# Optimization experiments

Hardware: AMD Instinct MI355X
Metric: run time of the kernel (lower is better)

The kernel has to match this reference:

```python
import jax, jax.numpy as jnp
import numpy as np

EPS = 1e-6  # cosine-similarity eps, as in pytorch3d chamfer_distance


def setup_inputs() -> dict:
    key = jax.random.key(0)
    k1, k2, k3, k4 = jax.random.split(key, 4)
    B, N, M, D = 4, 8192, 8192, 3
    return {
        "xyz1": jax.random.normal(k1, (B, N, D), dtype=jnp.float32),
        "xyz2": jax.random.normal(k2, (B, M, D), dtype=jnp.float32),
        "nxyz1": jax.random.normal(k3, (B, N, D), dtype=jnp.float32),
        "nxyz2": jax.random.normal(k4, (B, M, D), dtype=jnp.float32),
    }


def _pairwise_sqdist(x, y):
    # x: [B,N,D], y: [B,M,D] -> [B,N,M] squared euclidean distances
    x2 = jnp.sum(x * x, axis=-1)  # [B,N]
    y2 = jnp.sum(y * y, axis=-1)  # [B,M]
    xy = jnp.einsum("bnd,bmd->bnm", x, y)
    return x2[:, :, None] + y2[:, None, :] - 2.0 * xy


def _cos_sim(a, b):
    # cosine similarity along last axis with norm clamping (torch F.cosine_similarity style)
    na = jnp.maximum(jnp.linalg.norm(a, axis=-1), EPS)
    nb = jnp.maximum(jnp.linalg.norm(b, axis=-1), EPS)
    return jnp.sum(a * b, axis=-1) / (na * nb)


def reference(xyz1, xyz2, nxyz1, nxyz2):
    # pytorch3d chamfer_distance, point_reduction='mean', batch_reduction='mean'
    d = _pairwise_sqdist(xyz1, xyz2)          # [B,N,M]
    cham_x = jnp.min(d, axis=2)               # [B,N] nearest y for each x
    idx_x = jnp.argmin(d, axis=2)             # [B,N]
    cham_y = jnp.min(d, axis=1)               # [B,M] nearest x for each y
    idx_y = jnp.argmin(d, axis=1)             # [B,M]

    # point mean then batch mean == overall mean
    cham_dist = jnp.mean(cham_x) + jnp.mean(cham_y)

    # normal consistency: gather nearest-neighbor normals via argmin indices
    ny_for_x = jnp.take_along_axis(nxyz2, idx_x[:, :, None], axis=1)  # [B,N,3]
    nx_for_y = jnp.take_along_axis(nxyz1, idx_y[:, :, None], axis=1)  # [B,M,3]
    cham_norm_x = 1.0 - jnp.abs(_cos_sim(nxyz1, ny_for_x))            # [B,N]
    cham_norm_y = 1.0 - jnp.abs(_cos_sim(nxyz2, nx_for_y))            # [B,M]
    cham_normals = jnp.mean(cham_norm_x) + jnp.mean(cham_norm_y)

    return cham_dist, cham_normals
```

## Files before the change

kernel.cpp:

```cpp
#include <hip/hip_runtime.h>

#define CH_EPS 1e-6f
#define NPTS 8192
#define NB 4
#define NSEG 8
#define SEGSZ (NPTS / NSEG)
#define TILE 32
#define NTILE (SEGSZ / TILE)
#define CHSZ 16
#define NQT 4
#define QPW (32 * NQT)
#define QPB (4 * QPW)
#define NQ_TOT (2 * NB * NPTS)
#define BIGF 3.0e38f
#define CHMASK 0xFFFFFE00u

typedef _Float16 half8 __attribute__((ext_vector_type(8)));
typedef float floatx16 __attribute__((ext_vector_type(16)));

__device__ __forceinline__ unsigned mono(float f) {
    unsigned b = __float_as_uint(f);
    return (b & 0x80000000u) ? ~b : (b | 0x80000000u);
}
__device__ __forceinline__ unsigned mono_inv(unsigned u) {
    return (u & 0x80000000u) ? (u & 0x7FFFFFFFu) : ~u;
}

__global__ __launch_bounds__(256) void chamfer_partial(
    const float* __restrict__ xyz1, const float* __restrict__ xyz2,
    unsigned* __restrict__ part, float* __restrict__ out) {
    __shared__ half8 sA[SEGSZ + 1];

    const int tid = threadIdx.x;
    const int chq = blockIdx.x;
    const int seg = blockIdx.y;
    const int db = blockIdx.z;
    const int dir = db >> 2, b = db & 3;

    if (chq == 0 && seg == 0 && db == 0 && tid < 2) out[tid] = 0.0f;

    const float* Q = dir ? xyz2 : xyz1;
    const float* R = (dir ? xyz1 : xyz2) + ((size_t)b * NPTS + seg * SEGSZ) * 3;

    for (int k = tid; k < SEGSZ; k += 256) {
        float a = R[3 * k], c = R[3 * k + 1], e = R[3 * k + 2];
        float h = 0.5f * fmaf(a, a, fmaf(c, c, e * e));
        half8 v = {(_Float16)a, (_Float16)c, (_Float16)e, (_Float16)h,
                   (_Float16)0, (_Float16)0, (_Float16)0, (_Float16)0};
        sA[k] = v;
    }
    if (tid == 0) {
        half8 z = {(_Float16)0, (_Float16)0, (_Float16)0, (_Float16)0,
                   (_Float16)0, (_Float16)0, (_Float16)0, (_Float16)0};
        sA[SEGSZ] = z;
    }

    const int wave = tid >> 6, lane = tid & 63;
    const int n = lane & 31;
    const bool lohalf = lane < 32;
    const int qbase = chq * QPB + wave * QPW;

    half8 bfrag[NQT];
    float best[NQT];
#pragma unroll
    for (int qt = 0; qt < NQT; ++qt) {
        half8 v = {(_Float16)0, (_Float16)0, (_Float16)0, (_Float16)0,
                   (_Float16)0, (_Float16)0, (_Float16)0, (_Float16)0};
        if (lohalf) {
            const size_t off = ((size_t)b * NPTS + qbase + qt * 32 + n) * 3;
            v[0] = (_Float16)(-Q[off]);
            v[1] = (_Float16)(-Q[off + 1]);
            v[2] = (_Float16)(-Q[off + 2]);
            v[3] = (_Float16)1.0f;
        }
        bfrag[qt] = v;
        best[qt] = BIGF;
    }
    __syncthreads();

    const floatx16 zacc = {0};
    const unsigned gt0 = seg * NTILE;

    for (int rt = 0; rt < NTILE; ++rt) {
        const half8 af = sA[lohalf ? (rt * TILE + n) : SEGSZ];
        const unsigned gcl = (gt0 + rt) * 2;

        floatx16 d[NQT];
#pragma unroll
        for (int qt = 0; qt < NQT; ++qt)
            d[qt] = __builtin_amdgcn_mfma_f32_32x32x16_f16(
                af, bfrag[qt], zacc, 0, 0, 0);

#pragma unroll
        for (int qt = 0; qt < NQT; ++qt) {
            float lo = fminf(fminf(fminf(d[qt][0], d[qt][1]), fminf(d[qt][2], d[qt][3])),
                             fminf(fminf(d[qt][4], d[qt][5]), fminf(d[qt][6], d[qt][7])));
            float hi = fminf(fminf(fminf(d[qt][8], d[qt][9]), fminf(d[qt][10], d[qt][11])),
                             fminf(fminf(d[qt][12], d[qt][13]), fminf(d[qt][14], d[qt][15])));
            float kl = __uint_as_float((__float_as_uint(lo) & CHMASK) | gcl);
            float kh = __uint_as_float((__float_as_uint(hi) & CHMASK) | (gcl + 1));
            best[qt] = fminf(best[qt], fminf(kl, kh));
        }
    }

    const int qg = dir * (NB * NPTS) + b * NPTS + qbase;
#pragma unroll
    for (int qt = 0; qt < NQT; ++qt) {
        float v = best[qt];
        v = fminf(v, __shfl_xor(v, 32));
        if (lohalf) atomicMin(&part[qg + qt * 32 + n], mono(v));
    }
}

__global__ __launch_bounds__(256) void finalize_kernel(
    const float* __restrict__ xyz1, const float* __restrict__ xyz2,
    const float* __restrict__ nxyz1, const float* __restrict__ nxyz2,
    const unsigned* __restrict__ part, float* __restrict__ out) {
    __shared__ float red[2][4];

    const int tid = threadIdx.x;
    const int q = blockIdx.x * 256 + tid;
    const int dir = q >> 15;
    const int rem = q & 32767;
    const int b = rem >> 13;
    const int i = rem & 8191;

    const int c = (int)(mono_inv(part[q]) & 0x1FFu);

    const float* Q   = dir ? xyz2 : xyz1;
    const float* Rf  = dir ? xyz1 : xyz2;
    const float* NQp = dir ? nxyz2 : nxyz1;
    const float* NRp = dir ? nxyz1 : nxyz2;

    const size_t qoff = ((size_t)b * NPTS + i) * 3;
    const float x0 = Q[qoff], x1 = Q[qoff + 1], x2 = Q[qoff + 2];
    const float n0 = -x0, n1 = -x1, n2 = -x2;

    const float4* Rs = (const float4*)(Rf + ((size_t)b * NPTS + c * CHSZ) * 3);
    float btr = BIGF;
    int bj = 0;
#pragma unroll
    for (int g = 0; g < 4; ++g) {
        const float4 f0 = Rs[3 * g];
        const float4 f1 = Rs[3 * g + 1];
        const float4 f2 = Rs[3 * g + 2];
        const float px[4] = {f0.x, f0.w, f1.z, f2.y};
        const float py[4] = {f0.y, f1.x, f1.w, f2.z};
        const float pz[4] = {f0.z, f1.y, f2.x, f2.w};
#pragma unroll
        for (int u = 0; u < 4; ++u) {
            float h = 0.5f * fmaf(px[u], px[u], fmaf(py[u], py[u], pz[u] * pz[u]));
            float t = fmaf(n0, px[u], fmaf(n1, py[u], fmaf(n2, pz[u], h)));
            int j = 4 * g + u;
            if (t < btr) { btr = t; bj = j; }
        }
    }
    const int bi = c * CHSZ + bj;

    const size_t roff = ((size_t)b * NPTS + bi) * 3;
    const float y0 = Rf[roff], y1 = Rf[roff + 1], y2 = Rf[roff + 2];
    const float e0 = x0 - y0, e1 = x1 - y1, e2 = x2 - y2;
    float d = e0 * e0 + e1 * e1 + e2 * e2;

    const float a0 = NQp[qoff], a1 = NQp[qoff + 1], a2 = NQp[qoff + 2];
    const float c0 = NRp[roff], c1 = NRp[roff + 1], c2 = NRp[roff + 2];
    float na = sqrtf(a0 * a0 + a1 * a1 + a2 * a2);
    float nc = sqrtf(c0 * c0 + c1 * c1 + c2 * c2);
    float cs = (a0 * c0 + a1 * c1 + a2 * c2) /
               (fmaxf(na, CH_EPS) * fmaxf(nc, CH_EPS));
    float cn = 1.0f - fabsf(cs);

    for (int off = 32; off; off >>= 1) {
        d  += __shfl_down(d, off);
        cn += __shfl_down(cn, off);
    }
    const int lane = tid & 63, wv = tid >> 6;
    if (lane == 0) { red[0][wv] = d; red[1][wv] = cn; }
    __syncthreads();
    if (tid == 0) {
        float sd = red[0][0] + red[0][1] + red[0][2] + red[0][3];
        float sc = red[1][0] + red[1][1] + red[1][2] + red[1][3];
        const float inv = 1.0f / (float)(NB * NPTS);
        atomicAdd(out + 0, sd * inv);
        atomicAdd(out + 1, sc * inv);
    }
}

extern "C" void kernel_launch(void* const* d_in, const int* in_sizes, int n_in,
                              void* d_out, int out_size, void* d_ws, size_t ws_size,
                              hipStream_t stream) {
    const float* xyz1  = (const float*)d_in[0];
    const float* xyz2  = (const float*)d_in[1];
    const float* nxyz1 = (const float*)d_in[2];
    const float* nxyz2 = (const float*)d_in[3];
    float* out = (float*)d_out;
    unsigned* part = (unsigned*)d_ws;

    hipMemsetAsync(part, 0xFF, (size_t)NQ_TOT * sizeof(unsigned), stream);
    chamfer_partial<<<dim3(NPTS / QPB, NSEG, 2 * NB), dim3(256), 0, stream>>>(
        xyz1, xyz2, part, out);
    finalize_kernel<<<dim3(NQ_TOT / 256), dim3(256), 0, stream>>>(
        xyz1, xyz2, nxyz1, nxyz2, part, out);
}
```

Measured before the change: 106.0 us.

## Store per-segment partial minima instead of atomics; use 32-point chunk keys

Each segment now writes its per-query minimum key to its own slice of the workspace. The finalize kernel reduces the 16 slices itself, which removes the memset and the global atomicMin. Segments double to 16 for more blocks, and each key now encodes a 32-point chunk with an 8-bit index, folding both 32-row halves of the MFMA tile into a single min. The finalize kernel must now rescan 32 candidates per query and read 16 partial values, and the workspace grows by 16x. Negative distance keys still compare correctly under fminf.

After: 104.1 us. No clear change (-1.7%).

```diff
diff --git a/kernel.cpp b/kernel.cpp
--- a/kernel.cpp
+++ b/kernel.cpp
@@ -3,32 +3,24 @@
 #define CH_EPS 1e-6f
 #define NPTS 8192
 #define NB 4
-#define NSEG 8
+#define NSEG 16
 #define SEGSZ (NPTS / NSEG)
 #define TILE 32
 #define NTILE (SEGSZ / TILE)
-#define CHSZ 16
+#define CHSZ 32
 #define NQT 4
 #define QPW (32 * NQT)
 #define QPB (4 * QPW)
 #define NQ_TOT (2 * NB * NPTS)
 #define BIGF 3.0e38f
-#define CHMASK 0xFFFFFE00u
+#define CHMASK 0xFFFFFF00u
 
 typedef _Float16 half8 __attribute__((ext_vector_type(8)));
 typedef float floatx16 __attribute__((ext_vector_type(16)));
 
-__device__ __forceinline__ unsigned mono(float f) {
-    unsigned b = __float_as_uint(f);
-    return (b & 0x80000000u) ? ~b : (b | 0x80000000u);
-}
-__device__ __forceinline__ unsigned mono_inv(unsigned u) {
-    return (u & 0x80000000u) ? (u & 0x7FFFFFFFu) : ~u;
-}
-
 __global__ __launch_bounds__(256) void chamfer_partial(
     const float* __restrict__ xyz1, const float* __restrict__ xyz2,
-    unsigned* __restrict__ part, float* __restrict__ out) {
+    float* __restrict__ part, float* __restrict__ out) {
     __shared__ half8 sA[SEGSZ + 1];
 
     const int tid = threadIdx.x;
@@ -79,27 +71,22 @@
     __syncthreads();
 
     const floatx16 zacc = {0};
-    const unsigned gt0 = seg * NTILE;
+    const unsigned gc0 = seg * NTILE;
 
     for (int rt = 0; rt < NTILE; ++rt) {
         const half8 af = sA[lohalf ? (rt * TILE + n) : SEGSZ];
-        const unsigned gcl = (gt0 + rt) * 2;
-
-        floatx16 d[NQT];
-#pragma unroll
-        for (int qt = 0; qt < NQT; ++qt)
-            d[qt] = __builtin_amdgcn_mfma_f32_32x32x16_f16(
-                af, bfrag[qt], zacc, 0, 0, 0);
-
+        const unsigned gc = gc0 + rt;
 #pragma unroll
         for (int qt = 0; qt < NQT; ++qt) {
-            float lo = fminf(fminf(fminf(d[qt][0], d[qt][1]), fminf(d[qt][2], d[qt][3])),
-                             fminf(fminf(d[qt][4], d[qt][5]), fminf(d[qt][6], d[qt][7])));
-            float hi = fminf(fminf(fminf(d[qt][8], d[qt][9]), fminf(d[qt][10], d[qt][11])),
-                             fminf(fminf(d[qt][12], d[qt][13]), fminf(d[qt][14], d[qt][15])));
-            float kl = __uint_as_float((__float_as_uint(lo) & CHMASK) | gcl);
-            float kh = __uint_as_float((__float_as_uint(hi) & CHMASK) | (gcl + 1));
-            best[qt] = fminf(best[qt], fminf(kl, kh));
+            floatx16 d = __builtin_amdgcn_mfma_f32_32x32x16_f16(
+                af, bfrag[qt], zacc, 0, 0, 0);
+            float m0 = fminf(fminf(d[0], d[1]), fminf(d[2], d[3]));
+            float m1 = fminf(fminf(d[4], d[5]), fminf(d[6], d[7]));
+            float m2 = fminf(fminf(d[8], d[9]), fminf(d[10], d[11]));
+            float m3 = fminf(fminf(d[12], d[13]), fminf(d[14], d[15]));
+            float mn = fminf(fminf(m0, m1), fminf(m2, m3));
+            float key = __uint_as_float((__float_as_uint(mn) & CHMASK) | gc);
+            best[qt] = fminf(best[qt], key);
         }
     }
 
@@ -108,14 +95,14 @@
     for (int qt = 0; qt < NQT; ++qt) {
         float v = best[qt];
         v = fminf(v, __shfl_xor(v, 32));
-        if (lohalf) atomicMin(&part[qg + qt * 32 + n], mono(v));
+        if (lohalf) part[(size_t)seg * NQ_TOT + qg + qt * 32 + n] = v;
     }
 }
 
 __global__ __launch_bounds__(256) void finalize_kernel(
     const float* __restrict__ xyz1, const float* __restrict__ xyz2,
     const float* __restrict__ nxyz1, const float* __restrict__ nxyz2,
-    const unsigned* __restrict__ part, float* __restrict__ out) {
+    const float* __restrict__ part, float* __restrict__ out) {
     __shared__ float red[2][4];
 
     const int tid = threadIdx.x;
@@ -125,7 +112,10 @@
     const int b = rem >> 13;
     const int i = rem & 8191;
 
-    const int c = (int)(mono_inv(part[q]) & 0x1FFu);
+    float bt = part[q];
+#pragma unroll
+    for (int s = 1; s < NSEG; ++s) bt = fminf(bt, part[(size_t)s * NQ_TOT + q]);
+    const int c = (int)(__float_as_uint(bt) & 0xFFu);
 
     const float* Q   = dir ? xyz2 : xyz1;
     const float* Rf  = dir ? xyz1 : xyz2;
@@ -140,7 +130,7 @@
     float btr = BIGF;
     int bj = 0;
 #pragma unroll
-    for (int g = 0; g < 4; ++g) {
+    for (int g = 0; g < 8; ++g) {
         const float4 f0 = Rs[3 * g];
         const float4 f1 = Rs[3 * g + 1];
         const float4 f2 = Rs[3 * g + 2];
@@ -194,9 +184,8 @@
     const float* nxyz1 = (const float*)d_in[2];
     const float* nxyz2 = (const float*)d_in[3];
     float* out = (float*)d_out;
-    unsigned* part = (unsigned*)d_ws;
+    float* part = (float*)d_ws;
 
-    hipMemsetAsync(part, 0xFF, (size_t)NQ_TOT * sizeof(unsigned), stream);
     chamfer_partial<<<dim3(NPTS / QPB, NSEG, 2 * NB), dim3(256), 0, stream>>>(
         xyz1, xyz2, part, out);
     finalize_kernel<<<dim3(NQ_TOT / 256), dim3(256), 0, stream>>>(
```
